# Kernel tuning notes

Measured on AMD Instinct MI355X. Metric: run time of the kernel, lower is better.

The kernel has to match this reference:

```python
import jax, jax.numpy as jnp
import numpy as np
from jax import lax

N_FREE = 10
DT = 0.1
COMP = 4


def setup_inputs() -> dict:
    key = jax.random.key(0)
    kx, kw = jax.random.split(key)
    B, D = 256, 16384
    nodes = D // COMP  # 4096
    x = jax.random.normal(kx, (B, D), dtype=jnp.float32)
    # Hopfield-style node-coupling matrix (learned parameter), small init for stable relaxation
    W = jax.random.normal(kw, (nodes, nodes), dtype=jnp.float32) * 0.02
    return {"x": x, "W": W}


def reference(x, W):
    B, D = x.shape
    nodes = D // COMP
    # project scalar features to multivectors (B, nodes, comp)
    x_mv = x.reshape(B, nodes, COMP)
    W_sym = 0.5 * (W + W.T)  # symmetric coupling => well-defined energy

    def step(h, _):
        rho = jnp.tanh(h)                                      # (B, nodes, comp)
        drive = jnp.einsum('nm,bmc->bnc', W_sym, rho) + x_mv   # recurrent + input coupling
        grad_E = h - (1.0 - rho * rho) * drive                 # dE/dh
        return h - DT * grad_E, None

    h_free, _ = lax.scan(step, x_mv, None, length=N_FREE)
    return h_free[..., 0]  # scalar (grade-0) component, (B, nodes)
```

## Files before the change

### kernel.cpp

```cpp
#include <hip/hip_runtime.h>
#include <hip/hip_bf16.h>


#define BATCH   256
#define NODES   4096
#define MDIM    1024
#define KDIM    4096
#define DLEN    16384

typedef __attribute__((ext_vector_type(8))) __bf16 bf16x8;
typedef __attribute__((ext_vector_type(4))) float  f32x4;

static __device__ __forceinline__ unsigned short f32_to_bf16(float f) {
    unsigned int u = __float_as_uint(f);
    u += 0x7fffu + ((u >> 16) & 1u);
    return (unsigned short)(u >> 16);
}

__global__ __launch_bounds__(256)
void symw_kernel(const float* __restrict__ W, unsigned short* __restrict__ Wb) {
    __shared__ float Ta[64][64];
    __shared__ float Tb[64][65];
    const int tn = blockIdx.y, tm = blockIdx.x;
    const int c  = threadIdx.x & 63;
    const int r0 = threadIdx.x >> 6;
#pragma unroll
    for (int rr = 0; rr < 16; ++rr) {
        int r = r0 * 16 + rr;
        Ta[r][c] = W[(size_t)(tn * 64 + r) * 4096 + tm * 64 + c];
        Tb[r][c] = W[(size_t)(tm * 64 + r) * 4096 + tn * 64 + c];
    }
    __syncthreads();
#pragma unroll
    for (int rr = 0; rr < 16; ++rr) {
        int r = r0 * 16 + rr;
        float v = 0.5f * (Ta[r][c] + Tb[c][r]);
        Wb[(size_t)(tn * 64 + r) * 4096 + tm * 64 + c] = f32_to_bf16(v);
    }
}

__global__ __launch_bounds__(256)
void init_kernel(const float* __restrict__ x, float* __restrict__ h,
                 unsigned short* __restrict__ R0) {
    int idx = blockIdx.x * blockDim.x + threadIdx.x;
    int b = idx >> 12;
    int m = idx & 4095;
    f32x4 xv = *(const f32x4*)(x + (size_t)idx * 4);
    *(f32x4*)(h + (size_t)idx * 4) = xv;
#pragma unroll
    for (int c = 0; c < 4; ++c) {
        R0[((size_t)(b * 4 + c)) * (size_t)KDIM + m] = f32_to_bf16(tanhf(xv[c]));
    }
}

#define BM 64
#define BN 128
#define BK 64

__global__ __launch_bounds__(256, 2)
void step_kernel(const unsigned short* __restrict__ Rcur,
                 const unsigned short* __restrict__ Wb,
                 const float* __restrict__ x,
                 float* __restrict__ h,
                 unsigned short* __restrict__ Rnxt,
                 float* __restrict__ out) {
    __shared__ unsigned short As[BM * BK];
    __shared__ unsigned short Bs[BN * BK];

    const int tid  = threadIdx.x;
    const int bx   = blockIdx.x;
    const int by   = blockIdx.y;
    const int rowA0 = by * BM;
    const int rowB0 = bx * BN;

    const int w    = tid >> 6;
    const int lane = tid & 63;
    const int m0   = (w >> 1) * 32;
    const int n0   = (w & 1) * 64;
    const int lr   = lane & 15;
    const int lk   = lane >> 4;

    f32x4 acc[2][4];
#pragma unroll
    for (int mi = 0; mi < 2; ++mi)
#pragma unroll
        for (int ni = 0; ni < 4; ++ni)
            acc[mi][ni] = (f32x4){0.f, 0.f, 0.f, 0.f};

    for (int k0 = 0; k0 < KDIM; k0 += BK) {
#pragma unroll
        for (int j = 0; j < 2; ++j) {
            int chunk = tid + 256 * j;
            int row = chunk >> 3, cs = chunk & 7;
            int cg = cs ^ (row & 7);
            const unsigned short* g = Rcur + (size_t)(rowA0 + row) * KDIM + k0 + cg * 8;
            __builtin_amdgcn_global_load_lds(
                (const __attribute__((address_space(1))) void*)g,
                (__attribute__((address_space(3))) void*)(As + chunk * 8), 16, 0, 0);
        }
#pragma unroll
        for (int j = 0; j < 4; ++j) {
            int chunk = tid + 256 * j;
            int row = chunk >> 3, cs = chunk & 7;
            int cg = cs ^ (row & 7);
            const unsigned short* g = Wb + (size_t)(rowB0 + row) * KDIM + k0 + cg * 8;
            __builtin_amdgcn_global_load_lds(
                (const __attribute__((address_space(1))) void*)g,
                (__attribute__((address_space(3))) void*)(Bs + chunk * 8), 16, 0, 0);
        }
        __syncthreads();

#pragma unroll
        for (int kk = 0; kk < 2; ++kk) {
            bf16x8 a[2], b[4];
#pragma unroll
            for (int mi = 0; mi < 2; ++mi) {
                int row = m0 + mi * 16 + lr;
                int slot = (kk * 4 + lk) ^ (row & 7);
                a[mi] = *(const bf16x8*)(As + row * BK + slot * 8);
            }
#pragma unroll
            for (int ni = 0; ni < 4; ++ni) {
                int row = n0 + ni * 16 + lr;
                int slot = (kk * 4 + lk) ^ (row & 7);
                b[ni] = *(const bf16x8*)(Bs + row * BK + slot * 8);
            }
#pragma unroll
            for (int mi = 0; mi < 2; ++mi)
#pragma unroll
                for (int ni = 0; ni < 4; ++ni)
                    acc[mi][ni] = __builtin_amdgcn_mfma_f32_16x16x32_bf16(
                        a[mi], b[ni], acc[mi][ni], 0, 0, 0);
        }
        __syncthreads();
    }

#pragma unroll
    for (int mi = 0; mi < 2; ++mi) {
        int i0 = rowA0 + m0 + mi * 16 + lk * 4;
        int b  = i0 >> 2;
#pragma unroll
        for (int ni = 0; ni < 4; ++ni) {
            int n = rowB0 + n0 + ni * 16 + lr;
            size_t hidx = (size_t)b * DLEN + (size_t)n * 4;
            f32x4 h4 = *(const f32x4*)(h + hidx);
            f32x4 x4 = *(const f32x4*)(x + hidx);
            f32x4 hn;
#pragma unroll
            for (int r = 0; r < 4; ++r) {
                float hv   = h4[r];
                float rho  = tanhf(hv);
                float drive = acc[mi][ni][r] + x4[r];
                float hnew = 0.9f * hv + 0.1f * (1.0f - rho * rho) * drive;
                hn[r] = hnew;
                Rnxt[(size_t)(i0 + r) * KDIM + n] = f32_to_bf16(tanhf(hnew));
            }
            *(f32x4*)(h + hidx) = hn;
            if (out) out[(size_t)b * NODES + n] = hn[0];
        }
    }
}

extern "C" void kernel_launch(void* const* d_in, const int* in_sizes, int n_in,
                              void* d_out, int out_size, void* d_ws, size_t ws_size,
                              hipStream_t stream) {
    const float* x = (const float*)d_in[0];
    const float* W = (const float*)d_in[1];
    float* out = (float*)d_out;

    char* ws = (char*)d_ws;
    unsigned short* Wb = (unsigned short*)(ws);
    unsigned short* R0 = (unsigned short*)(ws + ((size_t)32 << 20));
    unsigned short* R1 = (unsigned short*)(ws + ((size_t)40 << 20));
    float*          h  = (float*)(ws + ((size_t)48 << 20));

    symw_kernel<<<dim3(64, 64), 256, 0, stream>>>(W, Wb);
    init_kernel<<<dim3(4096), 256, 0, stream>>>(x, h, R0);

    unsigned short* rc = R0;
    unsigned short* rn = R1;
    for (int s = 0; s < 10; ++s) {
        step_kernel<<<dim3(32, 16), 256, 0, stream>>>(
            rc, Wb, x, h, rn, (s == 9) ? out : nullptr);
        unsigned short* t = rc; rc = rn; rn = t;
    }
}
```

Before: 632.2 us.

## Double-buffer LDS tiles to overlap global loads with MFMA compute

```diff
diff --git a/kernel.cpp b/kernel.cpp
--- a/kernel.cpp
+++ b/kernel.cpp
@@ -64,8 +64,8 @@
                  float* __restrict__ h,
                  unsigned short* __restrict__ Rnxt,
                  float* __restrict__ out) {
-    __shared__ unsigned short As[BM * BK];
-    __shared__ unsigned short Bs[BN * BK];
+    __shared__ unsigned short As[2][BM * BK];
+    __shared__ unsigned short Bs[2][BN * BK];
 
     const int tid  = threadIdx.x;
     const int bx   = blockIdx.x;
@@ -80,6 +80,8 @@
     const int lr   = lane & 15;
     const int lk   = lane >> 4;
 
+    const int chA0 = tid,        chA1 = tid + 256;
+
     f32x4 acc[2][4];
 #pragma unroll
     for (int mi = 0; mi < 2; ++mi)
@@ -87,29 +89,45 @@
         for (int ni = 0; ni < 4; ++ni)
             acc[mi][ni] = (f32x4){0.f, 0.f, 0.f, 0.f};
 
-    for (int k0 = 0; k0 < KDIM; k0 += BK) {
-#pragma unroll
-        for (int j = 0; j < 2; ++j) {
-            int chunk = tid + 256 * j;
-            int row = chunk >> 3, cs = chunk & 7;
-            int cg = cs ^ (row & 7);
-            const unsigned short* g = Rcur + (size_t)(rowA0 + row) * KDIM + k0 + cg * 8;
-            __builtin_amdgcn_global_load_lds(
-                (const __attribute__((address_space(1))) void*)g,
-                (__attribute__((address_space(3))) void*)(As + chunk * 8), 16, 0, 0);
-        }
-#pragma unroll
-        for (int j = 0; j < 4; ++j) {
-            int chunk = tid + 256 * j;
-            int row = chunk >> 3, cs = chunk & 7;
-            int cg = cs ^ (row & 7);
-            const unsigned short* g = Wb + (size_t)(rowB0 + row) * KDIM + k0 + cg * 8;
-            __builtin_amdgcn_global_load_lds(
-                (const __attribute__((address_space(1))) void*)g,
-                (__attribute__((address_space(3))) void*)(Bs + chunk * 8), 16, 0, 0);
-        }
-        __syncthreads();
-
+#define STAGE(buf, k0)                                                          \
+    do {                                                                        \
+        _Pragma("unroll")                                                       \
+        for (int j = 0; j < 2; ++j) {                                           \
+            int chunk = tid + 256 * j;                                          \
+            int row = chunk >> 3, cs = chunk & 7;                               \
+            int cg = cs ^ (row & 7);                                            \
+            const unsigned short* g =                                           \
+                Rcur + (size_t)(rowA0 + row) * KDIM + (k0) + cg * 8;            \
+            __builtin_amdgcn_global_load_lds(                                   \
+                (const __attribute__((address_space(1))) void*)g,               \
+                (__attribute__((address_space(3))) void*)(As[buf] + chunk * 8), \
+                16, 0, 0);                                                      \
+        }                                                                       \
+        _Pragma("unroll")                                                       \
+        for (int j = 0; j < 4; ++j) {                                           \
+            int chunk = tid + 256 * j;                                          \
+            int row = chunk >> 3, cs = chunk & 7;                               \
+            int cg = cs ^ (row & 7);                                            \
+            const unsigned short* g =                                           \
+                Wb + (size_t)(rowB0 + row) * KDIM + (k0) + cg * 8;              \
+            __builtin_amdgcn_global_load_lds(                                   \
+                (const __attribute__((address_space(1))) void*)g,               \
+                (__attribute__((address_space(3))) void*)(Bs[buf] + chunk * 8), \
+                16, 0, 0);                                                      \
+        }                                                                       \
+    } while (0)
+
+    STAGE(0, 0);
+    asm volatile("s_waitcnt vmcnt(0)" ::: "memory");
+    __builtin_amdgcn_s_barrier();
+
+    const int NT = KDIM / BK;
+    for (int t = 0; t < NT; ++t) {
+        const int cur = t & 1;
+        if (t + 1 < NT) STAGE(cur ^ 1, (t + 1) * BK);
+
+        const unsigned short* Ab = As[cur];
+        const unsigned short* Bb = Bs[cur];
 #pragma unroll
         for (int kk = 0; kk < 2; ++kk) {
             bf16x8 a[2], b[4];
@@ -117,13 +135,13 @@
             for (int mi = 0; mi < 2; ++mi) {
                 int row = m0 + mi * 16 + lr;
                 int slot = (kk * 4 + lk) ^ (row & 7);
-                a[mi] = *(const bf16x8*)(As + row * BK + slot * 8);
+                a[mi] = *(const bf16x8*)(Ab + row * BK + slot * 8);
             }
 #pragma unroll
             for (int ni = 0; ni < 4; ++ni) {
                 int row = n0 + ni * 16 + lr;
                 int slot = (kk * 4 + lk) ^ (row & 7);
-                b[ni] = *(const bf16x8*)(Bs + row * BK + slot * 8);
+                b[ni] = *(const bf16x8*)(Bb + row * BK + slot * 8);
             }
 #pragma unroll
             for (int mi = 0; mi < 2; ++mi)
@@ -132,8 +150,10 @@
                     acc[mi][ni] = __builtin_amdgcn_mfma_f32_16x16x32_bf16(
                         a[mi], b[ni], acc[mi][ni], 0, 0, 0);
         }
-        __syncthreads();
-    }
+        asm volatile("s_waitcnt vmcnt(0)" ::: "memory");
+        __builtin_amdgcn_s_barrier();
+    }
+#undef STAGE
 
 #pragma unroll
     for (int mi = 0; mi < 2; ++mi) {
```

After: 667.8 us. 5.6% more time.
